# Optimization experiments

Measured on AMD Instinct MI355X. Metric: run time of the kernel, lower is better.

The kernel has to match this reference:

```python
import jax, jax.numpy as jnp
import numpy as np
import math

HIDDEN = 768
N_HEADS = 12
HEAD = HIDDEN // N_HEADS


def setup_inputs() -> dict:
    key = jax.random.key(0)
    k1, k2, k3, k4, k5 = jax.random.split(key, 5)
    x = jax.random.normal(k1, (2, 2048, HIDDEN), dtype=jnp.float32)
    s = 1.0 / math.sqrt(HIDDEN)
    W_qkv = jax.random.uniform(k2, (HIDDEN, 3 * HIDDEN), minval=-s, maxval=s, dtype=jnp.float32)
    b_qkv = jax.random.uniform(k3, (3 * HIDDEN,), minval=-s, maxval=s, dtype=jnp.float32)
    W_out = jax.random.uniform(k4, (HIDDEN, HIDDEN), minval=-s, maxval=s, dtype=jnp.float32)
    b_out = jax.random.uniform(k5, (HIDDEN,), minval=-s, maxval=s, dtype=jnp.float32)
    return {"x": x, "W_qkv": W_qkv, "b_qkv": b_qkv, "W_out": W_out, "b_out": b_out}


def reference(x, W_qkv, b_qkv, W_out, b_out):
    b, n, _ = x.shape
    qkv = x @ W_qkv + b_qkv                      # [b, n, 3H]
    q, k, v = jnp.split(qkv, 3, axis=-1)
    def heads(t):
        return t.reshape(b, n, N_HEADS, HEAD).transpose(0, 2, 1, 3)  # b h n l
    q, k, v = heads(q), heads(k), heads(v)
    scores = jnp.einsum('bhql,bhkl->bhqk', q, k) / math.sqrt(HEAD)
    mask = jnp.arange(n)[:, None] < jnp.arange(n)[None, :]  # True above diagonal
    scores = jnp.where(mask, jnp.float32(-10000.0), scores)
    attn = jax.nn.softmax(scores, axis=-1)
    out = jnp.einsum('bhqk,bhkl->bhql', attn, v)
    out = out.transpose(0, 2, 1, 3).reshape(b, n, HIDDEN)
    return out @ W_out + b_out
```

## Files before the change

### kernel.cpp

```cpp
#include <hip/hip_runtime.h>

typedef __attribute__((ext_vector_type(8))) short short8;
typedef __attribute__((ext_vector_type(4))) short short4v;
typedef __attribute__((ext_vector_type(4))) float floatx4;
typedef __attribute__((ext_vector_type(16))) float floatx16;

#define HIDDEN 768
#define NH 12
#define HD 64
#define SEQ 2048
#define BATCH 2
#define BHN (BATCH*NH)
#define MTOT (BATCH*SEQ)
#define NQKV (3*HIDDEN)
#define LDT 40
#define QSCALE 0.1803368801111204f

__device__ __forceinline__ short f2bf(float f) {
  union { float f; unsigned u; } v; v.f = f;
  unsigned r = v.u + 0x7FFFu + ((v.u >> 16) & 1u);
  return (short)(r >> 16);
}
__device__ __forceinline__ unsigned bfrne(float f) {
  unsigned u = __float_as_uint(f);
  return u + 0x7FFFu + ((u >> 16) & 1u);
}
__device__ __forceinline__ unsigned pk2(float a, float b) {
  return __builtin_amdgcn_perm(bfrne(b), bfrne(a), 0x07060302u);
}
__device__ __forceinline__ float bf2f(short s) {
  return __uint_as_float(((unsigned)(unsigned short)s) << 16);
}
__device__ __forceinline__ floatx4 mfma_bf16(short8 a, short8 b, floatx4 c) {
  return __builtin_amdgcn_mfma_f32_16x16x32_bf16(a, b, c, 0, 0, 0);
}
__device__ __forceinline__ floatx16 mfma32(short8 a, short8 b, floatx16 c) {
  return __builtin_amdgcn_mfma_f32_32x32x16_bf16(a, b, c, 0, 0, 0);
}
__device__ __forceinline__ short8 ld8(const short* p) {
  return *reinterpret_cast<const short8*>(p);
}

__global__ __launch_bounds__(256) void transpose_cvt(const float* __restrict__ W,
                                                     short* __restrict__ WT,
                                                     int K, int N) {
  __shared__ short t[64][72];
  int nb = blockIdx.x * 64, kb = blockIdx.y * 64;
  int tid = threadIdx.x;
  {
    int k  = tid >> 2;
    int n0 = (tid & 3) << 4;
    const float4* src = reinterpret_cast<const float4*>(W + (size_t)(kb + k) * N + nb + n0);
    #pragma unroll
    for (int c = 0; c < 4; ++c) {
      float4 v = src[c];
      t[n0 + c*4 + 0][k] = f2bf(v.x);
      t[n0 + c*4 + 1][k] = f2bf(v.y);
      t[n0 + c*4 + 2][k] = f2bf(v.z);
      t[n0 + c*4 + 3][k] = f2bf(v.w);
    }
  }
  __syncthreads();
  {
    int n  = tid >> 2;
    int k0 = (tid & 3) << 4;
    const short8* row = reinterpret_cast<const short8*>(&t[n][k0]);
    short8* dst = reinterpret_cast<short8*>(WT + (size_t)(nb + n) * K + kb + k0);
    dst[0] = row[0];
    dst[1] = row[1];
  }
}

__global__ __launch_bounds__(256) void cvt_x(const float* __restrict__ X,
                                             short* __restrict__ Xb) {
  int i = (blockIdx.x * 256 + threadIdx.x) * 8;
  const float4* s = reinterpret_cast<const float4*>(X + i);
  float4 v0 = s[0], v1 = s[1];
  short8 o;
  o[0] = f2bf(v0.x); o[1] = f2bf(v0.y); o[2] = f2bf(v0.z); o[3] = f2bf(v0.w);
  o[4] = f2bf(v1.x); o[5] = f2bf(v1.y); o[6] = f2bf(v1.z); o[7] = f2bf(v1.w);
  *reinterpret_cast<short8*>(Xb + i) = o;
}

__global__ __launch_bounds__(256) void gemm_qkv(const short* __restrict__ Xb,
                                                const short* __restrict__ WT,
                                                const float* __restrict__ bias,
                                                short* __restrict__ Qb,
                                                short* __restrict__ Kb,
                                                short* __restrict__ VTb) {
  __shared__ short As[128 * LDT];
  __shared__ short Bs[128 * LDT];
  int m0 = blockIdx.x * 128, n0 = blockIdx.y * 128;
  int tid = threadIdx.x;
  int lane = tid & 63, wv = tid >> 6;
  int wm = (wv >> 1) << 6, wn = (wv & 1) << 6;
  int quad = lane >> 4, l16 = lane & 15;
  floatx4 acc[4][4] = {};
  for (int kk = 0; kk < HIDDEN; kk += 32) {
    __syncthreads();
    #pragma unroll
    for (int c = 0; c < 2; ++c) {
      int idx = (tid + c * 256) * 8;
      int r = idx >> 5, col = idx & 31;
      *reinterpret_cast<short8*>(&As[r * LDT + col]) =
          ld8(Xb + (size_t)(m0 + r) * HIDDEN + kk + col);
      *reinterpret_cast<short8*>(&Bs[r * LDT + col]) =
          ld8(WT + (size_t)(n0 + r) * HIDDEN + kk + col);
    }
    __syncthreads();
    short8 af[4], bfr[4];
    #pragma unroll
    for (int i = 0; i < 4; ++i)
      af[i] = *reinterpret_cast<const short8*>(&As[(wm + i * 16 + l16) * LDT + quad * 8]);
    #pragma unroll
    for (int j = 0; j < 4; ++j)
      bfr[j] = *reinterpret_cast<const short8*>(&Bs[(wn + j * 16 + l16) * LDT + quad * 8]);
    #pragma unroll
    for (int i = 0; i < 4; ++i)
      #pragma unroll
      for (int j = 0; j < 4; ++j)
        acc[i][j] = mfma_bf16(af[i], bfr[j], acc[i][j]);
  }
  int colbase = n0 + wn;
  int part = colbase / HIDDEN;
  #pragma unroll
  for (int j = 0; j < 4; ++j) {
    int col = colbase + j * 16 + l16;
    float bs = bias[col];
    int rem = col - part * HIDDEN;
    int h = rem >> 6, d = rem & 63;
    #pragma unroll
    for (int i = 0; i < 4; ++i) {
      #pragma unroll
      for (int r = 0; r < 4; ++r) {
        int row = m0 + wm + i * 16 + quad * 4 + r;
        float v = acc[i][j][r] + bs;
        int bb = row >> 11, s = row & 2047;
        int bh = bb * NH + h;
        if (part == 0) {
          Qb[((size_t)bh * SEQ + s) * HD + d] = f2bf(v * QSCALE);
        } else if (part == 1) {
          Kb[((size_t)bh * SEQ + s) * HD + d] = f2bf(v);
        } else {
          VTb[((size_t)bh * HD + d) * SEQ + s] = f2bf(v);
        }
      }
    }
  }
}

__global__ __launch_bounds__(256, 4) void attn_partial(const short* __restrict__ Qb,
                                                       const short* __restrict__ Kb,
                                                       const short* __restrict__ VTb,
                                                       short* __restrict__ PO,
                                                       float* __restrict__ PM,
                                                       float* __restrict__ PL) {
  __shared__ __align__(16) char lds[32768];
  int blk = blockIdx.x;
  int cls = blk & 7;
  int j   = blk >> 3;
  int headsel = j / 40;
  int bh  = cls + 8 * headsel;
  int cidx = 39 - (j - headsel * 40);
  int qt, c;
  if (cidx < 4)       { qt = cidx;                  c = 0; }
  else if (cidx < 12) { qt = 4 + ((cidx - 4) >> 1); c = (cidx - 4) & 1; }
  else if (cidx < 24) { int t = cidx - 12; int q3 = t / 3; qt = 8 + q3; c = t - 3 * q3; }
  else                { int t = cidx - 24; qt = 12 + (t >> 2); c = t & 3; }
  int g = qt >> 2, p = qt & 3;
  int idx = bh * 40 + (g + 1) * (2 * g + p) + c;

  int nt  = 2 * qt + 2;
  int kt0 = c * 8;
  int kt1 = min(nt, kt0 + 8);
  int qb0 = qt * 128;

  int tid = threadIdx.x;
  int lane = tid & 63, wv = tid >> 6;
  int l31 = lane & 31, h = lane >> 5, x = lane & 7;
  const short* Qp = Qb + (size_t)bh * SEQ * HD;
  const short* Kp = Kb + (size_t)bh * SEQ * HD;
  const short* Vp = VTb + (size_t)bh * HD * SEQ;

  int qs  = qb0 + wv * 32 + l31;
  int qlo = qb0 + wv * 32;
  int qhi = qlo + 31;

  short8 bq[4];
  #pragma unroll
  for (int dc = 0; dc < 4; ++dc)
    bq[dc] = ld8(Qp + qs * HD + dc * 16 + h * 8);

  int sr = tid >> 2, scg = tid & 3;
  const short* kg = Kp + (kt0 * 64 + sr) * HD + scg * 16;
  const short* vg = Vp + (size_t)sr * SEQ + kt0 * 64 + scg * 16;
  int wbase = (sr << 7) | (((scg << 1) ^ (sr & 7)) << 4);

  int rbase[4];
  #pragma unroll
  for (int kc = 0; kc < 4; ++kc)
    rbase[kc] = (l31 << 7) | ((((kc << 1) | h) ^ x) << 4);

  {
    short8 k0 = ld8(kg), k1 = ld8(kg + 8);
    short8 v0 = ld8(vg), v1 = ld8(vg + 8);
    *reinterpret_cast<short8*>(lds + wbase)                = k0;
    *reinterpret_cast<short8*>(lds + (wbase ^ 16))         = k1;
    *reinterpret_cast<short8*>(lds + 16384 + wbase)        = v0;
    *reinterpret_cast<short8*>(lds + 16384 + (wbase ^ 16)) = v1;
  }
  __syncthreads();

  floatx16 o0 = {}, o1 = {};
  float m_run = -1e30f, l_run = 0.f;

  for (int kt = kt0; kt < kt1; ++kt) {
    int cur = (kt - kt0) & 1;
    int curK = cur * 8192, curV = 16384 + cur * 8192;
    int kb = kt * 64;
    bool have_next = (kt + 1 < kt1);

    short8 nk0, nk1, nv0, nv1;
    if (have_next) {
      kg += 64 * HD; vg += 64;
      nk0 = ld8(kg); nk1 = ld8(kg + 8);
      nv0 = ld8(vg); nv1 = ld8(vg + 8);
    }

    if (kb <= qhi) {
      floatx16 s0 = {}, s1 = {};
      #pragma unroll
      for (int kc = 0; kc < 4; ++kc) {
        short8 ka0 = *reinterpret_cast<const short8*>(lds + curK + rbase[kc]);
        short8 ka1 = *reinterpret_cast<const short8*>(lds + curK + 4096 + rbase[kc]);
        s0 = mfma32(ka0, bq[kc], s0);
        s1 = mfma32(ka1, bq[kc], s1);
      }
      if (kb + 63 > qlo) {
        #pragma unroll
        for (int r = 0; r < 16; ++r) {
          int kvr = kb + (r & 3) + 8 * (r >> 2) + 4 * h;
          s0[r] = (kvr > qs) ? -1e30f : s0[r];
          s1[r] = (kvr + 32 > qs) ? -1e30f : s1[r];
        }
      }
      float mloc = m_run;
      #pragma unroll
      for (int r = 0; r < 16; ++r) { mloc = fmaxf(mloc, s0[r]); mloc = fmaxf(mloc, s1[r]); }
      mloc = fmaxf(mloc, __shfl_xor(mloc, 32));
      float m_new = mloc;
      float alpha = __builtin_amdgcn_exp2f(m_run - m_new);
      float sloc = 0.f;
      #pragma unroll
      for (int r = 0; r < 16; ++r) {
        s0[r] = __builtin_amdgcn_exp2f(s0[r] - m_new); sloc += s0[r];
        s1[r] = __builtin_amdgcn_exp2f(s1[r] - m_new); sloc += s1[r];
      }
      sloc += __shfl_xor(sloc, 32);
      l_run = l_run * alpha + sloc;
      m_run = m_new;
      o0 *= alpha; o1 *= alpha;
      short8 pb[4];
      #pragma unroll
      for (int kvc = 0; kvc < 4; ++kvc) {
        int base = (kvc & 1) * 8;
        const floatx16& P = (kvc < 2) ? s0 : s1;
        unsigned e0 = pk2(P[base + 0], P[base + 1]);
        unsigned e1 = pk2(P[base + 2], P[base + 3]);
        unsigned f0 = pk2(P[base + 4], P[base + 5]);
        unsigned f1 = pk2(P[base + 6], P[base + 7]);
        unsigned k_0 = h ? f0 : e0, k_1 = h ? f1 : e1;
        unsigned s_0 = h ? e0 : f0, s_1 = h ? e1 : f1;
        unsigned r_0 = __shfl_xor((int)s_0, 32);
        unsigned r_1 = __shfl_xor((int)s_1, 32);
        union { unsigned u[4]; short8 v; } pbu;
        pbu.u[0] = h ? r_0 : k_0;
        pbu.u[1] = h ? r_1 : k_1;
        pbu.u[2] = h ? k_0 : r_0;
        pbu.u[3] = h ? k_1 : r_1;
        pb[kvc] = pbu.v;
      }
      #pragma unroll
      for (int kvc = 0; kvc < 4; ++kvc) {
        short8 va0 = *reinterpret_cast<const short8*>(lds + curV + rbase[kvc]);
        short8 va1 = *reinterpret_cast<const short8*>(lds + curV + 4096 + rbase[kvc]);
        o0 = mfma32(va0, pb[kvc], o0);
        o1 = mfma32(va1, pb[kvc], o1);
      }
    }

    if (have_next) {
      int nK = (cur ^ 1) * 8192, nV = 16384 + (cur ^ 1) * 8192;
      *reinterpret_cast<short8*>(lds + nK + wbase)        = nk0;
      *reinterpret_cast<short8*>(lds + nK + (wbase ^ 16)) = nk1;
      *reinterpret_cast<short8*>(lds + nV + wbase)        = nv0;
      *reinterpret_cast<short8*>(lds + nV + (wbase ^ 16)) = nv1;
    }
    __syncthreads();
  }

  int qloc = wv * 32 + l31;
  size_t pobase = (size_t)idx * 8192 + qloc * 64;
  #pragma unroll
  for (int dt = 0; dt < 2; ++dt) {
    #pragma unroll
    for (int cc = 0; cc < 4; ++cc) {
      int d = dt * 32 + 8 * cc + 4 * h;
      short4v w;
      #pragma unroll
      for (int r = 0; r < 4; ++r)
        w[r] = f2bf(dt ? o1[4 * cc + r] : o0[4 * cc + r]);
      *reinterpret_cast<short4v*>(PO + pobase + d) = w;
    }
  }
  if (h == 0) {
    PM[idx * 128 + qloc] = m_run;
    PL[idx * 128 + qloc] = l_run;
  }
}

__global__ __launch_bounds__(256) void attn_merge(const short* __restrict__ PO,
                                                  const float* __restrict__ PM,
                                                  const float* __restrict__ PL,
                                                  short* __restrict__ AO) {
  int blk = blockIdx.x;
  int bh = blk >> 4, qt = blk & 15;
  int g = qt >> 2, p = qt & 3;
  int base = bh * 40 + (g + 1) * (2 * g + p);
  int nc = g + 1;
  int tid = threadIdx.x;
  int q = tid >> 1, dh = (tid & 1) << 5;
  float mv[4];
  float M = -1e30f;
  for (int c = 0; c < nc; ++c) {
    mv[c] = PM[(base + c) * 128 + q];
    M = fmaxf(M, mv[c]);
  }
  float wsum = 0.f;
  float acc[32] = {};
  for (int c = 0; c < nc; ++c) {
    float w = __builtin_amdgcn_exp2f(mv[c] - M);
    wsum += PL[(base + c) * 128 + q] * w;
    const short8* po = reinterpret_cast<const short8*>(PO + (size_t)(base + c) * 8192 + q * 64 + dh);
    #pragma unroll
    for (int k = 0; k < 4; ++k) {
      short8 v = po[k];
      #pragma unroll
      for (int e = 0; e < 8; ++e)
        acc[k * 8 + e] += w * bf2f(v[e]);
    }
  }
  float inv = 1.f / wsum;
  int b = bh / NH, hh = bh % NH;
  int s = qt * 128 + q;
  short* dst = AO + ((size_t)(b * SEQ + s)) * HIDDEN + hh * HD + dh;
  #pragma unroll
  for (int k = 0; k < 4; ++k) {
    short8 w8;
    #pragma unroll
    for (int e = 0; e < 8; ++e)
      w8[e] = f2bf(acc[k * 8 + e] * inv);
    *reinterpret_cast<short8*>(dst + k * 8) = w8;
  }
}

__global__ __launch_bounds__(256) void gemm_out(const short* __restrict__ AO,
                                                const short* __restrict__ WT,
                                                const float* __restrict__ bias,
                                                float* __restrict__ out) {
  __shared__ short As[128 * LDT];
  __shared__ short Bs[128 * LDT];
  int m0 = blockIdx.x * 128, n0 = blockIdx.y * 128;
  int tid = threadIdx.x;
  int lane = tid & 63, wv = tid >> 6;
  int wm = (wv >> 1) << 6, wn = (wv & 1) << 6;
  int quad = lane >> 4, l16 = lane & 15;
  floatx4 acc[4][4] = {};
  for (int kk = 0; kk < HIDDEN; kk += 32) {
    __syncthreads();
    #pragma unroll
    for (int c = 0; c < 2; ++c) {
      int idx = (tid + c * 256) * 8;
      int r = idx >> 5, col = idx & 31;
      *reinterpret_cast<short8*>(&As[r * LDT + col]) =
          ld8(AO + (size_t)(m0 + r) * HIDDEN + kk + col);
      *reinterpret_cast<short8*>(&Bs[r * LDT + col]) =
          ld8(WT + (size_t)(n0 + r) * HIDDEN + kk + col);
    }
    __syncthreads();
    short8 af[4], bfr[4];
    #pragma unroll
    for (int i = 0; i < 4; ++i)
      af[i] = *reinterpret_cast<const short8*>(&As[(wm + i * 16 + l16) * LDT + quad * 8]);
    #pragma unroll
    for (int j = 0; j < 4; ++j)
      bfr[j] = *reinterpret_cast<const short8*>(&Bs[(wn + j * 16 + l16) * LDT + quad * 8]);
    #pragma unroll
    for (int i = 0; i < 4; ++i)
      #pragma unroll
      for (int j = 0; j < 4; ++j)
        acc[i][j] = mfma_bf16(af[i], bfr[j], acc[i][j]);
  }
  #pragma unroll
  for (int j = 0; j < 4; ++j) {
    int col = n0 + wn + j * 16 + l16;
    float bs = bias[col];
    #pragma unroll
    for (int i = 0; i < 4; ++i) {
      #pragma unroll
      for (int r = 0; r < 4; ++r) {
        int row = m0 + wm + i * 16 + quad * 4 + r;
        out[(size_t)row * HIDDEN + col] = acc[i][j][r] + bs;
      }
    }
  }
}

extern "C" void kernel_launch(void* const* d_in, const int* in_sizes, int n_in,
                              void* d_out, int out_size, void* d_ws, size_t ws_size,
                              hipStream_t stream) {
  const float* x    = (const float*)d_in[0];
  const float* Wqkv = (const float*)d_in[1];
  const float* bqkv = (const float*)d_in[2];
  const float* Wout = (const float*)d_in[3];
  const float* bout = (const float*)d_in[4];
  float* out = (float*)d_out;

  short* WqkvT = (short*)d_ws;
  short* WoutT = WqkvT + (size_t)NQKV * HIDDEN;
  short* Qb    = WoutT + (size_t)HIDDEN * HIDDEN;
  short* Kb    = Qb + (size_t)BHN * SEQ * HD;
  short* VTb   = Kb + (size_t)BHN * SEQ * HD;
  short* AO    = VTb + (size_t)BHN * SEQ * HD;
  short* Xb    = AO + (size_t)MTOT * HIDDEN;
  short* PO    = Xb;
  float* PM    = (float*)(PO + (size_t)960 * 8192);
  float* PL    = PM + 960 * 128;

  cvt_x<<<dim3(MTOT * HIDDEN / (256 * 8)), 256, 0, stream>>>(x, Xb);
  transpose_cvt<<<dim3(NQKV / 64, HIDDEN / 64), 256, 0, stream>>>(Wqkv, WqkvT, HIDDEN, NQKV);
  transpose_cvt<<<dim3(HIDDEN / 64, HIDDEN / 64), 256, 0, stream>>>(Wout, WoutT, HIDDEN, HIDDEN);
  gemm_qkv<<<dim3(MTOT / 128, NQKV / 128), 256, 0, stream>>>(Xb, WqkvT, bqkv, Qb, Kb, VTb);
  attn_partial<<<dim3(960), 256, 0, stream>>>(Qb, Kb, VTb, PO, PM, PL);
  attn_merge<<<dim3(BHN * 16), 256, 0, stream>>>(PO, PM, PL, AO);
  gemm_out<<<dim3(MTOT / 128, HIDDEN / 128), 256, 0, stream>>>(AO, WoutT, bout, out);
}
```

Before: 181.8 us.

## Load GEMM tiles with direct global-to-LDS copies and an XOR-swizzled LDS layout

The QKV and output-projection GEMMs now stage A and B tiles with global_load_lds, so 16-byte chunks go straight from global memory into shared memory without passing through registers. Padded rows (LDT 40) give way to unpadded 32-element rows, with an XOR swizzle on the chunk index applied at the global source address and again on the fragment reads to avoid bank conflicts. This cuts register pressure and load/store instructions in the main loop. Correctness now depends on the swizzle matching between writes and reads, and on the wave-contiguous LDS placement that global_load_lds requires.

```diff
diff --git a/kernel.cpp b/kernel.cpp
--- a/kernel.cpp
+++ b/kernel.cpp
@@ -13,7 +13,6 @@
 #define BHN (BATCH*NH)
 #define MTOT (BATCH*SEQ)
 #define NQKV (3*HIDDEN)
-#define LDT 40
 #define QSCALE 0.1803368801111204f
 
 __device__ __forceinline__ short f2bf(float f) {
@@ -39,6 +38,11 @@
 }
 __device__ __forceinline__ short8 ld8(const short* p) {
   return *reinterpret_cast<const short8*>(p);
+}
+__device__ __forceinline__ void glds16(const short* g, short* l) {
+  __builtin_amdgcn_global_load_lds(
+      (const __attribute__((address_space(1))) void*)g,
+      (__attribute__((address_space(3))) void*)l, 16, 0, 0);
 }
 
 __global__ __launch_bounds__(256) void transpose_cvt(const float* __restrict__ W,
@@ -88,33 +92,43 @@
                                                 short* __restrict__ Qb,
                                                 short* __restrict__ Kb,
                                                 short* __restrict__ VTb) {
-  __shared__ short As[128 * LDT];
-  __shared__ short Bs[128 * LDT];
+  __shared__ short As[128 * 32];
+  __shared__ short Bs[128 * 32];
   int m0 = blockIdx.x * 128, n0 = blockIdx.y * 128;
   int tid = threadIdx.x;
   int lane = tid & 63, wv = tid >> 6;
   int wm = (wv >> 1) << 6, wn = (wv & 1) << 6;
   int quad = lane >> 4, l16 = lane & 15;
+
+  int srow = lane >> 2;
+  int schunk = (lane & 3) ^ ((lane >> 3) & 3);
+  const short* ag0 = Xb + (size_t)(m0 + wv * 32 + srow) * HIDDEN + schunk * 8;
+  const short* ag1 = ag0 + 16 * HIDDEN;
+  const short* bg0 = WT + (size_t)(n0 + wv * 32 + srow) * HIDDEN + schunk * 8;
+  const short* bg1 = bg0 + 16 * HIDDEN;
+  short* lA0 = As + wv * 1024;
+  short* lB0 = Bs + wv * 1024;
+
+  int sw = ((l16 >> 1) & 3);
+  int aoff = (wm + l16) * 32 + ((quad ^ sw) << 3);
+  int boff = (wn + l16) * 32 + ((quad ^ sw) << 3);
+
   floatx4 acc[4][4] = {};
   for (int kk = 0; kk < HIDDEN; kk += 32) {
     __syncthreads();
-    #pragma unroll
-    for (int c = 0; c < 2; ++c) {
-      int idx = (tid + c * 256) * 8;
-      int r = idx >> 5, col = idx & 31;
-      *reinterpret_cast<short8*>(&As[r * LDT + col]) =
-          ld8(Xb + (size_t)(m0 + r) * HIDDEN + kk + col);
-      *reinterpret_cast<short8*>(&Bs[r * LDT + col]) =
-          ld8(WT + (size_t)(n0 + r) * HIDDEN + kk + col);
-    }
+    glds16(ag0, lA0);
+    glds16(ag1, lA0 + 512);
+    glds16(bg0, lB0);
+    glds16(bg1, lB0 + 512);
+    ag0 += 32; ag1 += 32; bg0 += 32; bg1 += 32;
     __syncthreads();
     short8 af[4], bfr[4];
     #pragma unroll
     for (int i = 0; i < 4; ++i)
-      af[i] = *reinterpret_cast<const short8*>(&As[(wm + i * 16 + l16) * LDT + quad * 8]);
+      af[i] = *reinterpret_cast<const short8*>(&As[aoff + i * 512]);
     #pragma unroll
     for (int j = 0; j < 4; ++j)
-      bfr[j] = *reinterpret_cast<const short8*>(&Bs[(wn + j * 16 + l16) * LDT + quad * 8]);
+      bfr[j] = *reinterpret_cast<const short8*>(&Bs[boff + j * 512]);
     #pragma unroll
     for (int i = 0; i < 4; ++i)
       #pragma unroll
@@ -368,33 +382,43 @@
                                                 const short* __restrict__ WT,
                                                 const float* __restrict__ bias,
                                                 float* __restrict__ out) {
-  __shared__ short As[128 * LDT];
-  __shared__ short Bs[128 * LDT];
+  __shared__ short As[128 * 32];
+  __shared__ short Bs[128 * 32];
   int m0 = blockIdx.x * 128, n0 = blockIdx.y * 128;
   int tid = threadIdx.x;
   int lane = tid & 63, wv = tid >> 6;
   int wm = (wv >> 1) << 6, wn = (wv & 1) << 6;
   int quad = lane >> 4, l16 = lane & 15;
+
+  int srow = lane >> 2;
+  int schunk = (lane & 3) ^ ((lane >> 3) & 3);
+  const short* ag0 = AO + (size_t)(m0 + wv * 32 + srow) * HIDDEN + schunk * 8;
+  const short* ag1 = ag0 + 16 * HIDDEN;
+  const short* bg0 = WT + (size_t)(n0 + wv * 32 + srow) * HIDDEN + schunk * 8;
+  const short* bg1 = bg0 + 16 * HIDDEN;
+  short* lA0 = As + wv * 1024;
+  short* lB0 = Bs + wv * 1024;
+
+  int sw = ((l16 >> 1) & 3);
+  int aoff = (wm + l16) * 32 + ((quad ^ sw) << 3);
+  int boff = (wn + l16) * 32 + ((quad ^ sw) << 3);
+
   floatx4 acc[4][4] = {};
   for (int kk = 0; kk < HIDDEN; kk += 32) {
     __syncthreads();
-    #pragma unroll
-    for (int c = 0; c < 2; ++c) {
-      int idx = (tid + c * 256) * 8;
-      int r = idx >> 5, col = idx & 31;
-      *reinterpret_cast<short8*>(&As[r * LDT + col]) =
-          ld8(AO + (size_t)(m0 + r) * HIDDEN + kk + col);
-      *reinterpret_cast<short8*>(&Bs[r * LDT + col]) =
-          ld8(WT + (size_t)(n0 + r) * HIDDEN + kk + col);
-    }
+    glds16(ag0, lA0);
+    glds16(ag1, lA0 + 512);
+    glds16(bg0, lB0);
+    glds16(bg1, lB0 + 512);
+    ag0 += 32; ag1 += 32; bg0 += 32; bg1 += 32;
     __syncthreads();
     short8 af[4], bfr[4];
     #pragma unroll
     for (int i = 0; i < 4; ++i)
-      af[i] = *reinterpret_cast<const short8*>(&As[(wm + i * 16 + l16) * LDT + quad * 8]);
+      af[i] = *reinterpret_cast<const short8*>(&As[aoff + i * 512]);
     #pragma unroll
     for (int j = 0; j < 4; ++j)
-      bfr[j] = *reinterpret_cast<const short8*>(&Bs[(wn + j * 16 + l16) * LDT + quad * 8]);
+      bfr[j] = *reinterpret_cast<const short8*>(&Bs[boff + j * 512]);
     #pragma unroll
     for (int i = 0; i < 4; ++i)
       #pragma unroll
```

Measured after the change: 163.3 us. 10.2% less time.

## Use direct global-to-LDS loads in GEMMs and attention, merge weight prep kernels

Applied to the files above, without the earlier changes.

Replaces register-staged global loads followed by LDS stores with global_load_lds direct transfers in both GEMMs and the attention K/V pipeline, using XOR-swizzled LDS layouts. The GEMM K-tile grows from 32 to 64, halving the barrier count. The attention prefetch into the other LDS buffer is now issued at the top of each iteration instead of being written back at the end. The two weight transpose kernels are merged into one launch. The risks are correctness of the swizzle mapping and reliance on an implicit wait before the barrier for the async LDS writes.

```diff
diff --git a/kernel.cpp b/kernel.cpp
--- a/kernel.cpp
+++ b/kernel.cpp
@@ -13,7 +13,6 @@
 #define BHN (BATCH*NH)
 #define MTOT (BATCH*SEQ)
 #define NQKV (3*HIDDEN)
-#define LDT 40
 #define QSCALE 0.1803368801111204f
 
 __device__ __forceinline__ short f2bf(float f) {
@@ -40,12 +39,22 @@
 __device__ __forceinline__ short8 ld8(const short* p) {
   return *reinterpret_cast<const short8*>(p);
 }
-
-__global__ __launch_bounds__(256) void transpose_cvt(const float* __restrict__ W,
-                                                     short* __restrict__ WT,
-                                                     int K, int N) {
+__device__ __forceinline__ void glds16(const short* g, short* l) {
+  __builtin_amdgcn_global_load_lds(
+      (const __attribute__((address_space(1))) void*)g,
+      (__attribute__((address_space(3))) void*)l, 16, 0, 0);
+}
+
+__global__ __launch_bounds__(256) void prep_w(const float* __restrict__ Wqkv,
+                                              const float* __restrict__ Wout,
+                                              short* __restrict__ WqkvT,
+                                              short* __restrict__ WoutT) {
   __shared__ short t[64][72];
-  int nb = blockIdx.x * 64, kb = blockIdx.y * 64;
+  int bx = blockIdx.x;
+  const float* W; short* WT; int N; int nb;
+  if (bx < 36) { W = Wqkv; WT = WqkvT; N = NQKV;   nb = bx * 64; }
+  else         { W = Wout; WT = WoutT; N = HIDDEN; nb = (bx - 36) * 64; }
+  int kb = blockIdx.y * 64;
   int tid = threadIdx.x;
   {
     int k  = tid >> 2;
@@ -65,7 +74,7 @@
     int n  = tid >> 2;
     int k0 = (tid & 3) << 4;
     const short8* row = reinterpret_cast<const short8*>(&t[n][k0]);
-    short8* dst = reinterpret_cast<short8*>(WT + (size_t)(nb + n) * K + kb + k0);
+    short8* dst = reinterpret_cast<short8*>(WT + (size_t)(nb + n) * HIDDEN + kb + k0);
     dst[0] = row[0];
     dst[1] = row[1];
   }
@@ -88,38 +97,50 @@
                                                 short* __restrict__ Qb,
                                                 short* __restrict__ Kb,
                                                 short* __restrict__ VTb) {
-  __shared__ short As[128 * LDT];
-  __shared__ short Bs[128 * LDT];
+  __shared__ short As[128 * 64];
+  __shared__ short Bs[128 * 64];
   int m0 = blockIdx.x * 128, n0 = blockIdx.y * 128;
   int tid = threadIdx.x;
   int lane = tid & 63, wv = tid >> 6;
   int wm = (wv >> 1) << 6, wn = (wv & 1) << 6;
   int quad = lane >> 4, l16 = lane & 15;
+
+  int l8 = lane & 7, lr = lane >> 3;
+  int cg = l8 ^ lr;
+  const short* ag = Xb + (size_t)(m0 + wv * 32 + lr) * HIDDEN + cg * 8;
+  const short* bg = WT + (size_t)(n0 + wv * 32 + lr) * HIDDEN + cg * 8;
+  short* lA = As + wv * 2048;
+  short* lB = Bs + wv * 2048;
+
+  int sw = l16 & 7;
+  int arow = (wm + l16) * 64, brow = (wn + l16) * 64;
+
   floatx4 acc[4][4] = {};
-  for (int kk = 0; kk < HIDDEN; kk += 32) {
+  for (int kk = 0; kk < HIDDEN; kk += 64) {
     __syncthreads();
     #pragma unroll
-    for (int c = 0; c < 2; ++c) {
-      int idx = (tid + c * 256) * 8;
-      int r = idx >> 5, col = idx & 31;
-      *reinterpret_cast<short8*>(&As[r * LDT + col]) =
-          ld8(Xb + (size_t)(m0 + r) * HIDDEN + kk + col);
-      *reinterpret_cast<short8*>(&Bs[r * LDT + col]) =
-          ld8(WT + (size_t)(n0 + r) * HIDDEN + kk + col);
-    }
+    for (int g = 0; g < 4; ++g) {
+      glds16(ag + g * 8 * HIDDEN, lA + g * 512);
+      glds16(bg + g * 8 * HIDDEN, lB + g * 512);
+    }
+    ag += 64; bg += 64;
     __syncthreads();
-    short8 af[4], bfr[4];
-    #pragma unroll
-    for (int i = 0; i < 4; ++i)
-      af[i] = *reinterpret_cast<const short8*>(&As[(wm + i * 16 + l16) * LDT + quad * 8]);
-    #pragma unroll
-    for (int j = 0; j < 4; ++j)
-      bfr[j] = *reinterpret_cast<const short8*>(&Bs[(wn + j * 16 + l16) * LDT + quad * 8]);
-    #pragma unroll
-    for (int i = 0; i < 4; ++i)
+    #pragma unroll
+    for (int kh = 0; kh < 2; ++kh) {
+      int co = (((kh << 2) | quad) ^ sw) << 3;
+      short8 af[4], bfr[4];
+      #pragma unroll
+      for (int i = 0; i < 4; ++i)
+        af[i] = *reinterpret_cast<const short8*>(&As[arow + i * 1024 + co]);
       #pragma unroll
       for (int j = 0; j < 4; ++j)
-        acc[i][j] = mfma_bf16(af[i], bfr[j], acc[i][j]);
+        bfr[j] = *reinterpret_cast<const short8*>(&Bs[brow + j * 1024 + co]);
+      #pragma unroll
+      for (int i = 0; i < 4; ++i)
+        #pragma unroll
+        for (int j = 0; j < 4; ++j)
+          acc[i][j] = mfma_bf16(af[i], bfr[j], acc[i][j]);
+    }
   }
   int colbase = n0 + wn;
   int part = colbase / HIDDEN;
@@ -191,24 +212,21 @@
   for (int dc = 0; dc < 4; ++dc)
     bq[dc] = ld8(Qp + qs * HD + dc * 16 + h * 8);
 
-  int sr = tid >> 2, scg = tid & 3;
-  const short* kg = Kp + (kt0 * 64 + sr) * HD + scg * 16;
-  const short* vg = Vp + (size_t)sr * SEQ + kt0 * 64 + scg * 16;
-  int wbase = (sr << 7) | (((scg << 1) ^ (sr & 7)) << 4);
+  int lr = lane >> 3;
+  int cgc = (lane & 7) ^ lr;
+  const short* kgl = Kp + (size_t)(kt0 * 64 + wv * 16 + lr) * HD + cgc * 8;
+  const short* vgl = Vp + (size_t)(wv * 16 + lr) * SEQ + kt0 * 64 + cgc * 8;
+  int wofs = wv * 2048;
 
   int rbase[4];
   #pragma unroll
   for (int kc = 0; kc < 4; ++kc)
     rbase[kc] = (l31 << 7) | ((((kc << 1) | h) ^ x) << 4);
 
-  {
-    short8 k0 = ld8(kg), k1 = ld8(kg + 8);
-    short8 v0 = ld8(vg), v1 = ld8(vg + 8);
-    *reinterpret_cast<short8*>(lds + wbase)                = k0;
-    *reinterpret_cast<short8*>(lds + (wbase ^ 16))         = k1;
-    *reinterpret_cast<short8*>(lds + 16384 + wbase)        = v0;
-    *reinterpret_cast<short8*>(lds + 16384 + (wbase ^ 16)) = v1;
-  }
+  glds16(kgl,            (short*)(lds + wofs));
+  glds16(kgl + 8 * HD,   (short*)(lds + wofs + 1024));
+  glds16(vgl,            (short*)(lds + 16384 + wofs));
+  glds16(vgl + 8 * SEQ,  (short*)(lds + 16384 + wofs + 1024));
   __syncthreads();
 
   floatx16 o0 = {}, o1 = {};
@@ -218,13 +236,14 @@
     int cur = (kt - kt0) & 1;
     int curK = cur * 8192, curV = 16384 + cur * 8192;
     int kb = kt * 64;
-    bool have_next = (kt + 1 < kt1);
-
-    short8 nk0, nk1, nv0, nv1;
-    if (have_next) {
-      kg += 64 * HD; vg += 64;
-      nk0 = ld8(kg); nk1 = ld8(kg + 8);
-      nv0 = ld8(vg); nv1 = ld8(vg + 8);
+
+    if (kt + 1 < kt1) {
+      kgl += 64 * HD; vgl += 64;
+      int nK = (cur ^ 1) * 8192, nV = 16384 + (cur ^ 1) * 8192;
+      glds16(kgl,           (short*)(lds + nK + wofs));
+      glds16(kgl + 8 * HD,  (short*)(lds + nK + wofs + 1024));
+      glds16(vgl,           (short*)(lds + nV + wofs));
+      glds16(vgl + 8 * SEQ, (short*)(lds + nV + wofs + 1024));
     }
 
     if (kb <= qhi) {
@@ -288,14 +307,6 @@
         o1 = mfma32(va1, pb[kvc], o1);
       }
     }
-
-    if (have_next) {
-      int nK = (cur ^ 1) * 8192, nV = 16384 + (cur ^ 1) * 8192;
-      *reinterpret_cast<short8*>(lds + nK + wbase)        = nk0;
-      *reinterpret_cast<short8*>(lds + nK + (wbase ^ 16)) = nk1;
-      *reinterpret_cast<short8*>(lds + nV + wbase)        = nv0;
-      *reinterpret_cast<short8*>(lds + nV + (wbase ^ 16)) = nv1;
-    }
     __syncthreads();
   }
 
@@ -368,38 +379,50 @@
                                                 const short* __restrict__ WT,
                                                 const float* __restrict__ bias,
                                                 float* __restrict__ out) {
-  __shared__ short As[128 * LDT];
-  __shared__ short Bs[128 * LDT];
+  __shared__ short As[128 * 64];
+  __shared__ short Bs[128 * 64];
   int m0 = blockIdx.x * 128, n0 = blockIdx.y * 128;
   int tid = threadIdx.x;
   int lane = tid & 63, wv = tid >> 6;
   int wm = (wv >> 1) << 6, wn = (wv & 1) << 6;
   int quad = lane >> 4, l16 = lane & 15;
+
+  int l8 = lane & 7, lr = lane >> 3;
+  int cg = l8 ^ lr;
+  const short* ag = AO + (size_t)(m0 + wv * 32 + lr) * HIDDEN + cg * 8;
+  const short* bg = WT + (size_t)(n0 + wv * 32 + lr) * HIDDEN + cg * 8;
+  short* lA = As + wv * 2048;
+  short* lB = Bs + wv * 2048;
+
+  int sw = l16 & 7;
+  int arow = (wm + l16) * 64, brow = (wn + l16) * 64;
+
   floatx4 acc[4][4] = {};
-  for (int kk = 0; kk < HIDDEN; kk += 32) {
+  for (int kk = 0; kk < HIDDEN; kk += 64) {
     __syncthreads();
     #pragma unroll
-    for (int c = 0; c < 2; ++c) {
-      int idx = (tid + c * 256) * 8;
-      int r = idx >> 5, col = idx & 31;
-      *reinterpret_cast<short8*>(&As[r * LDT + col]) =
-          ld8(AO + (size_t)(m0 + r) * HIDDEN + kk + col);
-      *reinterpret_cast<short8*>(&Bs[r * LDT + col]) =
-          ld8(WT + (size_t)(n0 + r) * HIDDEN + kk + col);
-    }
+    for (int g = 0; g < 4; ++g) {
+      glds16(ag + g * 8 * HIDDEN, lA + g * 512);
+      glds16(bg + g * 8 * HIDDEN, lB + g * 512);
+    }
+    ag += 64; bg += 64;
     __syncthreads();
-    short8 af[4], bfr[4];
-    #pragma unroll
-    for (int i = 0; i < 4; ++i)
-      af[i] = *reinterpret_cast<const short8*>(&As[(wm + i * 16 + l16) * LDT + quad * 8]);
-    #pragma unroll
-    for (int j = 0; j < 4; ++j)
-      bfr[j] = *reinterpret_cast<const short8*>(&Bs[(wn + j * 16 + l16) * LDT + quad * 8]);
-    #pragma unroll
-    for (int i = 0; i < 4; ++i)
+    #pragma unroll
+    for (int kh = 0; kh < 2; ++kh) {
+      int co = (((kh << 2) | quad) ^ sw) << 3;
+      short8 af[4], bfr[4];
+      #pragma unroll
+      for (int i = 0; i < 4; ++i)
+        af[i] = *reinterpret_cast<const short8*>(&As[arow + i * 1024 + co]);
       #pragma unroll
       for (int j = 0; j < 4; ++j)
-        acc[i][j] = mfma_bf16(af[i], bfr[j], acc[i][j]);
+        bfr[j] = *reinterpret_cast<const short8*>(&Bs[brow + j * 1024 + co]);
+      #pragma unroll
+      for (int i = 0; i < 4; ++i)
+        #pragma unroll
+        for (int j = 0; j < 4; ++j)
+          acc[i][j] = mfma_bf16(af[i], bfr[j], acc[i][j]);
+    }
   }
   #pragma unroll
   for (int j = 0; j < 4; ++j) {
@@ -438,8 +461,7 @@
   float* PL    = PM + 960 * 128;
 
   cvt_x<<<dim3(MTOT * HIDDEN / (256 * 8)), 256, 0, stream>>>(x, Xb);
-  transpose_cvt<<<dim3(NQKV / 64, HIDDEN / 64), 256, 0, stream>>>(Wqkv, WqkvT, HIDDEN, NQKV);
-  transpose_cvt<<<dim3(HIDDEN / 64, HIDDEN / 64), 256, 0, stream>>>(Wout, WoutT, HIDDEN, HIDDEN);
+  prep_w<<<dim3(48, 12), 256, 0, stream>>>(Wqkv, Wout, WqkvT, WoutT);
   gemm_qkv<<<dim3(MTOT / 128, NQKV / 128), 256, 0, stream>>>(Xb, WqkvT, bqkv, Qb, Kb, VTb);
   attn_partial<<<dim3(960), 256, 0, stream>>>(Qb, Kb, VTb, PO, PM, PL);
   attn_merge<<<dim3(BHN * 16), 256, 0, stream>>>(PO, PM, PL, AO);
```

New measurement: 169.1 us. -7.0%, faster.
